# Performance work log

Hardware: AMD Instinct MI355X
Metric: run time of the kernel (lower is better)

Reference implementation:

```python
import jax, jax.numpy as jnp
import numpy as np

B, S, H, E = 64, 1024, 256, 256

def setup_inputs() -> dict:
    key = jax.random.key(0)
    k = jax.random.split(key, 6)
    scale = 1.0 / np.sqrt(H)
    return {
        "data_alpha": jax.random.normal(k[0], (B, S, H), jnp.float32),
        "data_beta": jax.random.normal(k[1], (B, S, H), jnp.float32),
        "data_embed": jax.random.normal(k[2], (B, S, E), jnp.float32),
        "data_mask": jnp.ones((B, S), jnp.float32),
        "Wb": jax.random.normal(k[3], (E, H), jnp.float32) * scale,
        "bb": jnp.zeros((E,), jnp.float32),
        "Wa": jax.random.normal(k[4], (H,), jnp.float32) * scale,
        "ba": jnp.zeros((1,), jnp.float32),
    }

def reference(data_alpha, data_beta, data_embed, data_mask, Wb, bb, Wa, ba):
    # beta gates: tanh(Linear(H->E))  [B,S,E]
    beta_w = jnp.tanh(jnp.einsum('bsh,eh->bse', data_beta, Wb) + bb)
    # alpha logits: Linear(H->1)  [B,S]
    corr = jnp.einsum('bsh,h->bs', data_alpha, Wa) + ba
    attn = jnp.exp(corr)[:, None, :]                       # [B,1,S]
    seq = data_alpha.shape[1]
    flag = jnp.triu(jnp.ones((seq, seq), data_alpha.dtype))[None]  # j >= i
    ef = flag * data_mask[:, None, :]                      # [B,S,S]
    num = attn * ef                                        # [B,S,S]
    acc = jnp.sum(num, axis=-1, keepdims=True) + 1e-10     # [B,S,1]
    alpha = num / acc                                      # [B,S,S]
    ew = beta_w * data_embed                               # [B,S,E]
    return jnp.einsum('bij,bje->bie', alpha, ew)           # [B,S,E]
```

## Files before the change

### kernel.cpp

```cpp
#include <hip/hip_runtime.h>
#include <hip/hip_bf16.h>

#define B_ 64
#define S_ 1024
#define H_ 256
#define E_ 256
#define C_ 16
#define CS_ 64

typedef __attribute__((ext_vector_type(8))) __bf16 bf16x8;
typedef __attribute__((ext_vector_type(4))) __bf16 bf16x4;
typedef __attribute__((ext_vector_type(4))) float f32x4;

__global__ __launch_bounds__(256) void k0_wb_bf16(const float* __restrict__ Wb,
                                                  __bf16* __restrict__ WbBf) {
    int i = blockIdx.x * 256 + threadIdx.x;
    float4 v = ((const float4*)Wb)[i];
    bf16x4 b;
    b[0] = (__bf16)v.x; b[1] = (__bf16)v.y;
    b[2] = (__bf16)v.z; b[3] = (__bf16)v.w;
    ((bf16x4*)WbBf)[i] = b;
}

__global__ __launch_bounds__(256, 4) void k2_fused(
        const float* __restrict__ alpha, const float* __restrict__ beta,
        const float* __restrict__ embed, const float* __restrict__ mask,
        const __bf16* __restrict__ WbBf, const float* __restrict__ bb,
        const float* __restrict__ Wa,    const float* __restrict__ ba,
        float* __restrict__ w, float* __restrict__ chunkTot, float* __restrict__ t) {
    __shared__ float red[4 * E_];
    __shared__ float wsh[CS_];

    const int tid = threadIdx.x;
    const int wv = tid >> 6, lane = tid & 63;
    const int l15 = lane & 15, q = lane >> 4;
    const int m0 = blockIdx.x * CS_;

    {
        const int pr = tid >> 2, pc = tid & 3;
        const int m = m0 + pr;
        const float4* ar = (const float4*)(alpha + (size_t)m * H_ + pc * 64);
        const float4* wr = (const float4*)(Wa + pc * 64);
        float p = 0.f;
        #pragma unroll
        for (int i = 0; i < 16; ++i) {
            float4 a = ar[i], v = wr[i];
            p += a.x * v.x + a.y * v.y + a.z * v.z + a.w * v.w;
        }
        p += __shfl_xor(p, 1, 64);
        p += __shfl_xor(p, 2, 64);
        if (pc == 0) {
            float wm = __expf(p + ba[0]) * mask[m];
            wsh[pr] = wm;
            w[m] = wm;
        }
    }
    __syncthreads();

    const float*  Arow = beta + (size_t)(m0 + wv * 16 + l15) * H_ + q * 8;
    const __bf16* Brow = WbBf + (size_t)l15 * H_ + q * 8;
    f32x4 acc[16];
    #pragma unroll
    for (int i = 0; i < 16; ++i) acc[i] = (f32x4){0.f, 0.f, 0.f, 0.f};

    #pragma unroll 2
    for (int kc = 0; kc < 8; ++kc) {
        float4 a0 = *(const float4*)(Arow + kc * 32);
        float4 a1 = *(const float4*)(Arow + kc * 32 + 4);
        bf16x8 af;
        af[0] = (__bf16)a0.x; af[1] = (__bf16)a0.y;
        af[2] = (__bf16)a0.z; af[3] = (__bf16)a0.w;
        af[4] = (__bf16)a1.x; af[5] = (__bf16)a1.y;
        af[6] = (__bf16)a1.z; af[7] = (__bf16)a1.w;
        #pragma unroll
        for (int et = 0; et < 16; ++et) {
            bf16x8 bf = *(const bf16x8*)(Brow + (size_t)et * 16 * H_ + kc * 32);
            acc[et] = __builtin_amdgcn_mfma_f32_16x16x32_bf16(af, bf, acc[et], 0, 0, 0);
        }
    }

    float wmr[4];
    #pragma unroll
    for (int r = 0; r < 4; ++r) wmr[r] = wsh[wv * 16 + q * 4 + r];

    #pragma unroll
    for (int et = 0; et < 16; ++et) {
        const int e = et * 16 + l15;
        const float bbe = bb[e];
        float tv[4];
        #pragma unroll
        for (int r = 0; r < 4; ++r) {
            const int m = m0 + wv * 16 + q * 4 + r;
            float x = acc[et][r] + bbe;
            x = fminf(fmaxf(x, -15.f), 15.f);
            float ex = __expf(2.f * x);
            float th = (ex - 1.f) / (ex + 1.f);
            tv[r] = wmr[r] * th * embed[(size_t)m * E_ + e];
        }
        float s3 = tv[3];
        float s2 = tv[2] + s3;
        float s1 = tv[1] + s2;
        float s0 = tv[0] + s1;
        float g  = s0;
        float g1 = __shfl_down(g, 16, 64);
        float g2 = __shfl_down(g, 32, 64);
        float g3 = __shfl_down(g, 48, 64);
        float addG = (q < 3 ? g1 : 0.f) + (q < 2 ? g2 : 0.f) + (q < 1 ? g3 : 0.f);
        if (q == 0) red[wv * E_ + e] = g + addG;
        acc[et][0] = s0 + addG;
        acc[et][1] = s1 + addG;
        acc[et][2] = s2 + addG;
        acc[et][3] = s3 + addG;
    }
    __syncthreads();

    #pragma unroll
    for (int et = 0; et < 16; ++et) {
        const int e = et * 16 + l15;
        float wa = 0.f;
        #pragma unroll
        for (int d = 1; d < 4; ++d)
            if (wv + d < 4) wa += red[(wv + d) * E_ + e];
        #pragma unroll
        for (int r = 0; r < 4; ++r) {
            const int m = m0 + wv * 16 + q * 4 + r;
            t[(size_t)m * E_ + e] = acc[et][r] + wa;
        }
    }
    const float ct = red[tid] + red[E_ + tid] + red[2 * E_ + tid] + red[3 * E_ + tid];
    chunkTot[(size_t)blockIdx.x * E_ + tid] = ct;
}

__global__ __launch_bounds__(256) void k3b_scan(
        const float* __restrict__ w, const float* __restrict__ chunkTot,
        float* __restrict__ chunkOff, float* __restrict__ invDen) {
    const int tid = threadIdx.x;
    const int b = blockIdx.x;

    float acc = 0.f;
    #pragma unroll
    for (int c = C_ - 1; c >= 0; --c) {
        chunkOff[((size_t)b * C_ + c) * E_ + tid] = acc;
        acc += chunkTot[((size_t)b * C_ + c) * E_ + tid];
    }

    float4 w4 = *(const float4*)(w + b * S_ + tid * 4);
    float tot = w4.x + w4.y + w4.z + w4.w;
    int lane = tid & 63, wv = tid >> 6;
    float suf = tot;
    #pragma unroll
    for (int off = 1; off < 64; off <<= 1) {
        float o = __shfl_down(suf, off, 64);
        if (lane + off < 64) suf += o;
    }
    __shared__ float wsum[4];
    if (lane == 0) wsum[wv] = suf;
    __syncthreads();
    float waveOff = 0.f;
    for (int j = wv + 1; j < 4; ++j) waveOff += wsum[j];
    float after = (suf - tot) + waveOff;
    float s3 = w4.w + after;
    float s2 = w4.z + s3;
    float s1 = w4.y + s2;
    float s0 = w4.x + s1;
    float4 inv = { 1.f / (s0 + 1e-10f), 1.f / (s1 + 1e-10f),
                   1.f / (s2 + 1e-10f), 1.f / (s3 + 1e-10f) };
    *(float4*)(invDen + b * S_ + tid * 4) = inv;
}

__global__ __launch_bounds__(256) void k3c_finish(
        float* __restrict__ t, const float* __restrict__ chunkOff,
        const float* __restrict__ invDen) {
    const int blk = blockIdx.x;
    const int b = blk >> 4, c = blk & 15;
    const int tid = threadIdx.x;
    float4* tp = (float4*)(t + ((size_t)b * S_ + c * CS_) * E_);
    const float4* co = (const float4*)(chunkOff + (size_t)blk * E_);
    const float* iv = invDen + b * S_ + c * CS_;
    #pragma unroll
    for (int i = 0; i < 16; ++i) {
        const int idx = i * 256 + tid;
        const int row = idx >> 6;
        const int e4 = idx & 63;
        float4 v = tp[idx];
        float4 o = co[e4];
        float s = iv[row];
        v.x = (v.x + o.x) * s;
        v.y = (v.y + o.y) * s;
        v.z = (v.z + o.z) * s;
        v.w = (v.w + o.w) * s;
        tp[idx] = v;
    }
}

extern "C" void kernel_launch(void* const* d_in, const int* in_sizes, int n_in,
                              void* d_out, int out_size, void* d_ws, size_t ws_size,
                              hipStream_t stream) {
    const float* alpha = (const float*)d_in[0];
    const float* beta  = (const float*)d_in[1];
    const float* embed = (const float*)d_in[2];
    const float* mask  = (const float*)d_in[3];
    const float* Wb    = (const float*)d_in[4];
    const float* bb    = (const float*)d_in[5];
    const float* Wa    = (const float*)d_in[6];
    const float* ba    = (const float*)d_in[7];

    float* t = (float*)d_out;

    char* ws = (char*)d_ws;
    float*  w        = (float*)ws;
    float*  chunkTot = (float*)(ws + (256 << 10));
    float*  chunkOff = (float*)(ws + (256 << 10) + (1 << 20));
    float*  invDen   = (float*)(ws + (256 << 10) + (2 << 20));
    __bf16* WbBf     = (__bf16*)(ws + (512 << 10) + (2 << 20));

    k0_wb_bf16<<<E_ * H_ / 1024, 256, 0, stream>>>(Wb, WbBf);
    k2_fused<<<B_ * C_, 256, 0, stream>>>(alpha, beta, embed, mask, WbBf, bb, Wa, ba,
                                          w, chunkTot, t);
    k3b_scan<<<B_, 256, 0, stream>>>(w, chunkTot, chunkOff, invDen);
    k3c_finish<<<B_ * C_, 256, 0, stream>>>(t, chunkOff, invDen);
}
```

Baseline: 303.0 us.

## Fuse scan and finish into cooperative grid-synced kernel, stage Wb in LDS

Makes the main kernel cooperative. After computing per-chunk partial sums it does a grid-wide sync, then computes chunk offsets and denominators locally and writes final outputs directly. This removes the separate scan and finish kernels and the extra read-modify-write of the output. The Wb tiles are also staged through padded LDS per k-chunk instead of being read from global memory by every wave. The cost is a grid barrier, added block syncs in the MFMA loop, and a fallback to the old path if cooperative launch is not supported.

```diff
diff --git a/kernel.cpp b/kernel.cpp
--- a/kernel.cpp
+++ b/kernel.cpp
@@ -1,5 +1,8 @@
 #include <hip/hip_runtime.h>
 #include <hip/hip_bf16.h>
+#include <hip/hip_cooperative_groups.h>
+
+namespace cg = cooperative_groups;
 
 #define B_ 64
 #define S_ 1024
@@ -8,6 +11,8 @@
 #define C_ 16
 #define CS_ 64
 
+#define LDSB_STRIDE 40
+
 typedef __attribute__((ext_vector_type(8))) __bf16 bf16x8;
 typedef __attribute__((ext_vector_type(4))) __bf16 bf16x4;
 typedef __attribute__((ext_vector_type(4))) float f32x4;
@@ -16,25 +21,31 @@
                                                   __bf16* __restrict__ WbBf) {
     int i = blockIdx.x * 256 + threadIdx.x;
     float4 v = ((const float4*)Wb)[i];
-    bf16x4 b;
-    b[0] = (__bf16)v.x; b[1] = (__bf16)v.y;
-    b[2] = (__bf16)v.z; b[3] = (__bf16)v.w;
-    ((bf16x4*)WbBf)[i] = b;
-}
-
-__global__ __launch_bounds__(256, 4) void k2_fused(
+    bf16x4 bv;
+    bv[0] = (__bf16)v.x; bv[1] = (__bf16)v.y;
+    bv[2] = (__bf16)v.z; bv[3] = (__bf16)v.w;
+    ((bf16x4*)WbBf)[i] = bv;
+}
+
+template <bool COOP>
+__global__ __launch_bounds__(256, 4) void k2_main(
         const float* __restrict__ alpha, const float* __restrict__ beta,
         const float* __restrict__ embed, const float* __restrict__ mask,
         const __bf16* __restrict__ WbBf, const float* __restrict__ bb,
         const float* __restrict__ Wa,    const float* __restrict__ ba,
-        float* __restrict__ w, float* __restrict__ chunkTot, float* __restrict__ t) {
+        float* __restrict__ chunkTot, float* __restrict__ wChunkSum,
+        float* __restrict__ w, float* __restrict__ t) {
+    __shared__ __bf16 ldsB[E_ * LDSB_STRIDE];
     __shared__ float red[4 * E_];
     __shared__ float wsh[CS_];
+    __shared__ float wsuf[CS_];
 
     const int tid = threadIdx.x;
     const int wv = tid >> 6, lane = tid & 63;
     const int l15 = lane & 15, q = lane >> 4;
-    const int m0 = blockIdx.x * CS_;
+    const int blk = blockIdx.x;
+    const int bat = blk >> 4, c = blk & 15;
+    const int m0 = blk * CS_;
 
     {
         const int pr = tid >> 2, pc = tid & 3;
@@ -52,21 +63,39 @@
         if (pc == 0) {
             float wm = __expf(p + ba[0]) * mask[m];
             wsh[pr] = wm;
-            w[m] = wm;
+            if constexpr (!COOP) w[m] = wm;
         }
     }
     __syncthreads();
-
-    const float*  Arow = beta + (size_t)(m0 + wv * 16 + l15) * H_ + q * 8;
-    const __bf16* Brow = WbBf + (size_t)l15 * H_ + q * 8;
+    if constexpr (COOP) {
+        if (tid < 64) {
+            float v = wsh[tid];
+            #pragma unroll
+            for (int off = 32; off; off >>= 1) v += __shfl_xor(v, off, 64);
+            if (tid == 0) wChunkSum[blk] = v;
+        }
+    }
+
+    const float* Arow = beta + (size_t)(m0 + wv * 16 + l15) * H_ + q * 8;
     f32x4 acc[16];
     #pragma unroll
     for (int i = 0; i < 16; ++i) acc[i] = (f32x4){0.f, 0.f, 0.f, 0.f};
 
-    #pragma unroll 2
+    const int se = tid >> 2;
+    const int sk = (tid & 3) * 8;
+
     for (int kc = 0; kc < 8; ++kc) {
         float4 a0 = *(const float4*)(Arow + kc * 32);
         float4 a1 = *(const float4*)(Arow + kc * 32 + 4);
+
+        #pragma unroll
+        for (int pass = 0; pass < 4; ++pass) {
+            int e = pass * 64 + se;
+            bf16x8 bv = *(const bf16x8*)(WbBf + (size_t)e * H_ + kc * 32 + sk);
+            *(bf16x8*)(ldsB + e * LDSB_STRIDE + sk) = bv;
+        }
+        __syncthreads();
+
         bf16x8 af;
         af[0] = (__bf16)a0.x; af[1] = (__bf16)a0.y;
         af[2] = (__bf16)a0.z; af[3] = (__bf16)a0.w;
@@ -74,9 +103,10 @@
         af[6] = (__bf16)a1.z; af[7] = (__bf16)a1.w;
         #pragma unroll
         for (int et = 0; et < 16; ++et) {
-            bf16x8 bf = *(const bf16x8*)(Brow + (size_t)et * 16 * H_ + kc * 32);
+            bf16x8 bf = *(const bf16x8*)(ldsB + (et * 16 + l15) * LDSB_STRIDE + q * 8);
             acc[et] = __builtin_amdgcn_mfma_f32_16x16x32_bf16(af, bf, acc[et], 0, 0, 0);
         }
+        __syncthreads();
     }
 
     float wmr[4];
@@ -114,21 +144,70 @@
     }
     __syncthreads();
 
+    const float ct = red[tid] + red[E_ + tid] + red[2 * E_ + tid] + red[3 * E_ + tid];
+    chunkTot[(size_t)blk * E_ + tid] = ct;
     #pragma unroll
     for (int et = 0; et < 16; ++et) {
         const int e = et * 16 + l15;
         float wa = 0.f;
-        #pragma unroll
-        for (int d = 1; d < 4; ++d)
-            if (wv + d < 4) wa += red[(wv + d) * E_ + e];
-        #pragma unroll
-        for (int r = 0; r < 4; ++r) {
-            const int m = m0 + wv * 16 + q * 4 + r;
-            t[(size_t)m * E_ + e] = acc[et][r] + wa;
-        }
-    }
-    const float ct = red[tid] + red[E_ + tid] + red[2 * E_ + tid] + red[3 * E_ + tid];
-    chunkTot[(size_t)blockIdx.x * E_ + tid] = ct;
+        if (wv < 3) wa += red[(wv + 1) * E_ + e];
+        if (wv < 2) wa += red[(wv + 2) * E_ + e];
+        if (wv < 1) wa += red[(wv + 3) * E_ + e];
+        acc[et][0] += wa; acc[et][1] += wa;
+        acc[et][2] += wa; acc[et][3] += wa;
+    }
+
+    if constexpr (!COOP) {
+        #pragma unroll
+        for (int et = 0; et < 16; ++et) {
+            const int e = et * 16 + l15;
+            #pragma unroll
+            for (int r = 0; r < 4; ++r) {
+                const int m = m0 + wv * 16 + q * 4 + r;
+                t[(size_t)m * E_ + e] = acc[et][r];
+            }
+        }
+        return;
+    } else {
+        __threadfence();
+        cg::this_grid().sync();
+        __threadfence();
+
+        float off = 0.f;
+        for (int cc = c + 1; cc < C_; ++cc)
+            off += chunkTot[((size_t)(bat * C_ + cc)) * E_ + tid];
+        red[tid] = off;
+
+        float wtail = 0.f;
+        for (int cc = c + 1; cc < C_; ++cc)
+            wtail += wChunkSum[bat * C_ + cc];
+
+        if (tid < 64) wsuf[tid] = wsh[tid];
+        __syncthreads();
+        for (int d = 1; d < 64; d <<= 1) {
+            float v = 0.f;
+            if (tid < 64 && tid + d < 64) v = wsuf[tid + d];
+            __syncthreads();
+            if (tid < 64) wsuf[tid] += v;
+            __syncthreads();
+        }
+
+        float inv[4];
+        #pragma unroll
+        for (int r = 0; r < 4; ++r)
+            inv[r] = 1.f / (wsuf[wv * 16 + q * 4 + r] + wtail + 1e-10f);
+
+        #pragma unroll
+        for (int et = 0; et < 16; ++et) {
+            const int e = et * 16 + l15;
+            const float oe = red[e];
+            #pragma unroll
+            for (int r = 0; r < 4; ++r) {
+                const int m = m0 + wv * 16 + q * 4 + r;
+                t[(size_t)m * E_ + e] = (acc[et][r] + oe) * inv[r];
+            }
+        }
+    }
 }
 
 __global__ __launch_bounds__(256) void k3b_scan(
@@ -193,6 +272,8 @@
     }
 }
 
+static int g_coop = -1;
+
 extern "C" void kernel_launch(void* const* d_in, const int* in_sizes, int n_in,
                               void* d_out, int out_size, void* d_ws, size_t ws_size,
                               hipStream_t stream) {
@@ -201,22 +282,44 @@
     const float* embed = (const float*)d_in[2];
     const float* mask  = (const float*)d_in[3];
     const float* Wb    = (const float*)d_in[4];
-    const float* bb    = (const float*)d_in[5];
+    const float* bbp   = (const float*)d_in[5];
     const float* Wa    = (const float*)d_in[6];
-    const float* ba    = (const float*)d_in[7];
+    const float* bap   = (const float*)d_in[7];
 
     float* t = (float*)d_out;
 
     char* ws = (char*)d_ws;
-    float*  w        = (float*)ws;
-    float*  chunkTot = (float*)(ws + (256 << 10));
-    float*  chunkOff = (float*)(ws + (256 << 10) + (1 << 20));
-    float*  invDen   = (float*)(ws + (256 << 10) + (2 << 20));
-    __bf16* WbBf     = (__bf16*)(ws + (512 << 10) + (2 << 20));
+    float*  chunkTot  = (float*)ws;
+    float*  wChunkSum = (float*)(ws + (1 << 20));
+    float*  w         = (float*)(ws + (1 << 20) + (16 << 10));
+    float*  chunkOff  = (float*)(ws + (1 << 20) + (16 << 10) + (256 << 10));
+    float*  invDen    = (float*)(ws + (2 << 20) + (16 << 10) + (256 << 10));
+    __bf16* WbBf      = (__bf16*)(ws + (2 << 20) + (16 << 10) + (512 << 10));
+
+    if (g_coop < 0) {
+        int dev = 0;
+        hipGetDevice(&dev);
+        int attr = 0;
+        hipDeviceGetAttribute(&attr, hipDeviceAttributeCooperativeLaunch, dev);
+        int nb = 0;
+        hipOccupancyMaxActiveBlocksPerMultiprocessor(&nb, k2_main<true>, 256, 0);
+        g_coop = (attr != 0 && nb >= 4) ? 1 : 0;
+    }
 
     k0_wb_bf16<<<E_ * H_ / 1024, 256, 0, stream>>>(Wb, WbBf);
-    k2_fused<<<B_ * C_, 256, 0, stream>>>(alpha, beta, embed, mask, WbBf, bb, Wa, ba,
-                                          w, chunkTot, t);
+
+    if (g_coop == 1) {
+        void* args[] = { (void*)&alpha, (void*)&beta, (void*)&embed, (void*)&mask,
+                         (void*)&WbBf, (void*)&bbp, (void*)&Wa, (void*)&bap,
+                         (void*)&chunkTot, (void*)&wChunkSum, (void*)&w, (void*)&t };
+        hipError_t e = hipLaunchCooperativeKernel(k2_main<true>, dim3(B_ * C_),
+                                                  dim3(256), args, 0u, stream);
+        if (e == hipSuccess) return;
+        g_coop = 0;
+    }
+
+    k2_main<false><<<B_ * C_, 256, 0, stream>>>(alpha, beta, embed, mask, WbBf, bbp,
+                                                Wa, bap, chunkTot, wChunkSum, w, t);
     k3b_scan<<<B_, 256, 0, stream>>>(w, chunkTot, chunkOff, invDen);
     k3c_finish<<<B_ * C_, 256, 0, stream>>>(t, chunkOff, invDen);
 }
```

Measured after the change: 262.6 us. 13.3% less time.

## Fuse chunk scan and normalization into main kernel with per-E-group sequential sweep

Applied to the files above, without the earlier changes.

Restructures the pipeline into two kernels. A prep kernel now computes the exp-logit weights alongside the Wb bf16 conversion. The main kernel assigns each block one batch and a 32-wide E slice and walks the sequence chunks from end to start, carrying the running suffix sum in LDS. It computes the denominator scan in-block and writes the final normalized output directly. This removes the chunk totals/offsets buffers, the separate scan kernel, and the extra read-modify-write pass over the output. In exchange, beta is re-read once per E group, relying on cache to absorb it. Each block also processes its chunks serially with barriers, which reduces the parallelism available inside a block.

```diff
diff --git a/kernel.cpp b/kernel.cpp
--- a/kernel.cpp
+++ b/kernel.cpp
@@ -5,191 +5,213 @@
 #define S_ 1024
 #define H_ 256
 #define E_ 256
-#define C_ 16
-#define CS_ 64
+
+#define EG_ 32
+#define LDSB_ST 264
+#define CH_ 128
+#define NCH_ 8
 
 typedef __attribute__((ext_vector_type(8))) __bf16 bf16x8;
 typedef __attribute__((ext_vector_type(4))) __bf16 bf16x4;
 typedef __attribute__((ext_vector_type(4))) float f32x4;
 
-__global__ __launch_bounds__(256) void k0_wb_bf16(const float* __restrict__ Wb,
-                                                  __bf16* __restrict__ WbBf) {
-    int i = blockIdx.x * 256 + threadIdx.x;
-    float4 v = ((const float4*)Wb)[i];
-    bf16x4 b;
-    b[0] = (__bf16)v.x; b[1] = (__bf16)v.y;
-    b[2] = (__bf16)v.z; b[3] = (__bf16)v.w;
-    ((bf16x4*)WbBf)[i] = b;
+__global__ __launch_bounds__(256) void k0_prep(
+        const float* __restrict__ alpha, const float* __restrict__ mask,
+        const float* __restrict__ Wa,    const float* __restrict__ ba,
+        const float* __restrict__ Wb,    __bf16* __restrict__ WbBf,
+        float* __restrict__ w) {
+    const int tid = threadIdx.x, blk = blockIdx.x;
+    if (blk < 64) {
+        int i = blk * 256 + tid;
+        float4 v = ((const float4*)Wb)[i];
+        bf16x4 bv;
+        bv[0] = (__bf16)v.x; bv[1] = (__bf16)v.y;
+        bv[2] = (__bf16)v.z; bv[3] = (__bf16)v.w;
+        ((bf16x4*)WbBf)[i] = bv;
+    }
+    const int pr = tid >> 2, pc = tid & 3;
+    const int m = blk * 64 + pr;
+    const float4* ar = (const float4*)(alpha + (size_t)m * H_ + pc * 64);
+    const float4* wr = (const float4*)(Wa + pc * 64);
+    float p = 0.f;
+    #pragma unroll
+    for (int i = 0; i < 16; ++i) {
+        float4 a = ar[i], v = wr[i];
+        p += a.x * v.x + a.y * v.y + a.z * v.z + a.w * v.w;
+    }
+    p += __shfl_xor(p, 1, 64);
+    p += __shfl_xor(p, 2, 64);
+    if (pc == 0) w[m] = __expf(p + ba[0]) * mask[m];
 }
 
-__global__ __launch_bounds__(256, 4) void k2_fused(
-        const float* __restrict__ alpha, const float* __restrict__ beta,
-        const float* __restrict__ embed, const float* __restrict__ mask,
+__global__ __launch_bounds__(512, 4) void k2_main(
+        const float* __restrict__ beta, const float* __restrict__ embed,
         const __bf16* __restrict__ WbBf, const float* __restrict__ bb,
-        const float* __restrict__ Wa,    const float* __restrict__ ba,
-        float* __restrict__ w, float* __restrict__ chunkTot, float* __restrict__ t) {
-    __shared__ float red[4 * E_];
-    __shared__ float wsh[CS_];
+        const float* __restrict__ w, float* __restrict__ t) {
+    __shared__ __bf16 ldsB[EG_ * LDSB_ST];
+    __shared__ float wsLds[S_];
+    __shared__ float ivLds[S_];
+    __shared__ float red[8 * EG_];
+    __shared__ float run[EG_];
+    __shared__ float wsum[4];
 
     const int tid = threadIdx.x;
     const int wv = tid >> 6, lane = tid & 63;
     const int l15 = lane & 15, q = lane >> 4;
-    const int m0 = blockIdx.x * CS_;
-
+    const int blk = blockIdx.x;
+    const int b  = (blk & 7) * 8 + (blk >> 6);
+    const int eg = (blk >> 3) & 7;
+
+    if (tid < 256)
+        *(float4*)(wsLds + tid * 4) = *(const float4*)(w + b * S_ + tid * 4);
     {
-        const int pr = tid >> 2, pc = tid & 3;
-        const int m = m0 + pr;
-        const float4* ar = (const float4*)(alpha + (size_t)m * H_ + pc * 64);
-        const float4* wr = (const float4*)(Wa + pc * 64);
-        float p = 0.f;
+        const int e = tid >> 4, ks = (tid & 15) * 16;
+        const __bf16* src = WbBf + (size_t)(eg * EG_ + e) * H_ + ks;
+        *(bf16x8*)(ldsB + e * LDSB_ST + ks)     = *(const bf16x8*)(src);
+        *(bf16x8*)(ldsB + e * LDSB_ST + ks + 8) = *(const bf16x8*)(src + 8);
+    }
+    if (tid < EG_) run[tid] = 0.f;
+    __syncthreads();
+
+    {
+        float w0 = 0, w1 = 0, w2 = 0, w3 = 0, tot = 0, suf = 0;
+        const int sl = tid & 63, sw = tid >> 6;
+        if (tid < 256) {
+            w0 = wsLds[tid * 4];     w1 = wsLds[tid * 4 + 1];
+            w2 = wsLds[tid * 4 + 2]; w3 = wsLds[tid * 4 + 3];
+            tot = w0 + w1 + w2 + w3;
+            suf = tot;
+            #pragma unroll
+            for (int off = 1; off < 64; off <<= 1) {
+                float o = __shfl_down(suf, off, 64);
+                if (sl + off < 64) suf += o;
+            }
+            if (sl == 0) wsum[sw] = suf;
+        }
+        __syncthreads();
+        if (tid < 256) {
+            float waveOff = 0.f;
+            for (int j = sw + 1; j < 4; ++j) waveOff += wsum[j];
+            float after = (suf - tot) + waveOff;
+            float s3 = w3 + after, s2 = w2 + s3, s1 = w1 + s2, s0 = w0 + s1;
+            ivLds[tid * 4]     = 1.f / (s0 + 1e-10f);
+            ivLds[tid * 4 + 1] = 1.f / (s1 + 1e-10f);
+            ivLds[tid * 4 + 2] = 1.f / (s2 + 1e-10f);
+            ivLds[tid * 4 + 3] = 1.f / (s3 + 1e-10f);
+        }
+        __syncthreads();
+    }
+
+    const float bb0 = bb[eg * EG_ + l15];
+    const float bb1 = bb[eg * EG_ + 16 + l15];
+
+    for (int c = NCH_ - 1; c >= 0; --c) {
+        const int rbase = c * CH_ + wv * 16;
+        const float* Ar = beta + (size_t)(b * S_ + rbase + l15) * H_ + q * 8;
+
+        f32x4 acc0 = {0.f, 0.f, 0.f, 0.f}, acc1 = {0.f, 0.f, 0.f, 0.f};
         #pragma unroll
-        for (int i = 0; i < 16; ++i) {
-            float4 a = ar[i], v = wr[i];
-            p += a.x * v.x + a.y * v.y + a.z * v.z + a.w * v.w;
-        }
-        p += __shfl_xor(p, 1, 64);
-        p += __shfl_xor(p, 2, 64);
-        if (pc == 0) {
-            float wm = __expf(p + ba[0]) * mask[m];
-            wsh[pr] = wm;
-            w[m] = wm;
-        }
-    }
-    __syncthreads();
-
-    const float*  Arow = beta + (size_t)(m0 + wv * 16 + l15) * H_ + q * 8;
-    const __bf16* Brow = WbBf + (size_t)l15 * H_ + q * 8;
-    f32x4 acc[16];
-    #pragma unroll
-    for (int i = 0; i < 16; ++i) acc[i] = (f32x4){0.f, 0.f, 0.f, 0.f};
-
-    #pragma unroll 2
-    for (int kc = 0; kc < 8; ++kc) {
-        float4 a0 = *(const float4*)(Arow + kc * 32);
-        float4 a1 = *(const float4*)(Arow + kc * 32 + 4);
-        bf16x8 af;
-        af[0] = (__bf16)a0.x; af[1] = (__bf16)a0.y;
-        af[2] = (__bf16)a0.z; af[3] = (__bf16)a0.w;
-        af[4] = (__bf16)a1.x; af[5] = (__bf16)a1.y;
-        af[6] = (__bf16)a1.z; af[7] = (__bf16)a1.w;
-        #pragma unroll
-        for (int et = 0; et < 16; ++et) {
-            bf16x8 bf = *(const bf16x8*)(Brow + (size_t)et * 16 * H_ + kc * 32);
-            acc[et] = __builtin_amdgcn_mfma_f32_16x16x32_bf16(af, bf, acc[et], 0, 0, 0);
-        }
-    }
-
-    float wmr[4];
-    #pragma unroll
-    for (int r = 0; r < 4; ++r) wmr[r] = wsh[wv * 16 + q * 4 + r];
-
-    #pragma unroll
-    for (int et = 0; et < 16; ++et) {
-        const int e = et * 16 + l15;
-        const float bbe = bb[e];
-        float tv[4];
-        #pragma unroll
-        for (int r = 0; r < 4; ++r) {
-            const int m = m0 + wv * 16 + q * 4 + r;
-            float x = acc[et][r] + bbe;
-            x = fminf(fmaxf(x, -15.f), 15.f);
-            float ex = __expf(2.f * x);
-            float th = (ex - 1.f) / (ex + 1.f);
-            tv[r] = wmr[r] * th * embed[(size_t)m * E_ + e];
-        }
-        float s3 = tv[3];
-        float s2 = tv[2] + s3;
-        float s1 = tv[1] + s2;
-        float s0 = tv[0] + s1;
-        float g  = s0;
-        float g1 = __shfl_down(g, 16, 64);
-        float g2 = __shfl_down(g, 32, 64);
-        float g3 = __shfl_down(g, 48, 64);
-        float addG = (q < 3 ? g1 : 0.f) + (q < 2 ? g2 : 0.f) + (q < 1 ? g3 : 0.f);
-        if (q == 0) red[wv * E_ + e] = g + addG;
-        acc[et][0] = s0 + addG;
-        acc[et][1] = s1 + addG;
-        acc[et][2] = s2 + addG;
-        acc[et][3] = s3 + addG;
-    }
-    __syncthreads();
-
-    #pragma unroll
-    for (int et = 0; et < 16; ++et) {
-        const int e = et * 16 + l15;
-        float wa = 0.f;
-        #pragma unroll
-        for (int d = 1; d < 4; ++d)
-            if (wv + d < 4) wa += red[(wv + d) * E_ + e];
-        #pragma unroll
-        for (int r = 0; r < 4; ++r) {
-            const int m = m0 + wv * 16 + q * 4 + r;
-            t[(size_t)m * E_ + e] = acc[et][r] + wa;
-        }
-    }
-    const float ct = red[tid] + red[E_ + tid] + red[2 * E_ + tid] + red[3 * E_ + tid];
-    chunkTot[(size_t)blockIdx.x * E_ + tid] = ct;
-}
-
-__global__ __launch_bounds__(256) void k3b_scan(
-        const float* __restrict__ w, const float* __restrict__ chunkTot,
-        float* __restrict__ chunkOff, float* __restrict__ invDen) {
-    const int tid = threadIdx.x;
-    const int b = blockIdx.x;
-
-    float acc = 0.f;
-    #pragma unroll
-    for (int c = C_ - 1; c >= 0; --c) {
-        chunkOff[((size_t)b * C_ + c) * E_ + tid] = acc;
-        acc += chunkTot[((size_t)b * C_ + c) * E_ + tid];
-    }
-
-    float4 w4 = *(const float4*)(w + b * S_ + tid * 4);
-    float tot = w4.x + w4.y + w4.z + w4.w;
-    int lane = tid & 63, wv = tid >> 6;
-    float suf = tot;
-    #pragma unroll
-    for (int off = 1; off < 64; off <<= 1) {
-        float o = __shfl_down(suf, off, 64);
-        if (lane + off < 64) suf += o;
-    }
-    __shared__ float wsum[4];
-    if (lane == 0) wsum[wv] = suf;
-    __syncthreads();
-    float waveOff = 0.f;
-    for (int j = wv + 1; j < 4; ++j) waveOff += wsum[j];
-    float after = (suf - tot) + waveOff;
-    float s3 = w4.w + after;
-    float s2 = w4.z + s3;
-    float s1 = w4.y + s2;
-    float s0 = w4.x + s1;
-    float4 inv = { 1.f / (s0 + 1e-10f), 1.f / (s1 + 1e-10f),
-                   1.f / (s2 + 1e-10f), 1.f / (s3 + 1e-10f) };
-    *(float4*)(invDen + b * S_ + tid * 4) = inv;
-}
-
-__global__ __launch_bounds__(256) void k3c_finish(
-        float* __restrict__ t, const float* __restrict__ chunkOff,
-        const float* __restrict__ invDen) {
-    const int blk = blockIdx.x;
-    const int b = blk >> 4, c = blk & 15;
-    const int tid = threadIdx.x;
-    float4* tp = (float4*)(t + ((size_t)b * S_ + c * CS_) * E_);
-    const float4* co = (const float4*)(chunkOff + (size_t)blk * E_);
-    const float* iv = invDen + b * S_ + c * CS_;
-    #pragma unroll
-    for (int i = 0; i < 16; ++i) {
-        const int idx = i * 256 + tid;
-        const int row = idx >> 6;
-        const int e4 = idx & 63;
-        float4 v = tp[idx];
-        float4 o = co[e4];
-        float s = iv[row];
-        v.x = (v.x + o.x) * s;
-        v.y = (v.y + o.y) * s;
-        v.z = (v.z + o.z) * s;
-        v.w = (v.w + o.w) * s;
-        tp[idx] = v;
+        for (int kc = 0; kc < 8; ++kc) {
+            float4 a0 = *(const float4*)(Ar + kc * 32);
+            float4 a1 = *(const float4*)(Ar + kc * 32 + 4);
+            bf16x8 af;
+            af[0] = (__bf16)a0.x; af[1] = (__bf16)a0.y;
+            af[2] = (__bf16)a0.z; af[3] = (__bf16)a0.w;
+            af[4] = (__bf16)a1.x; af[5] = (__bf16)a1.y;
+            af[6] = (__bf16)a1.z; af[7] = (__bf16)a1.w;
+            bf16x8 bf0 = *(const bf16x8*)(ldsB + l15 * LDSB_ST + kc * 32 + q * 8);
+            bf16x8 bf1 = *(const bf16x8*)(ldsB + (16 + l15) * LDSB_ST + kc * 32 + q * 8);
+            acc0 = __builtin_amdgcn_mfma_f32_16x16x32_bf16(af, bf0, acc0, 0, 0, 0);
+            acc1 = __builtin_amdgcn_mfma_f32_16x16x32_bf16(af, bf1, acc1, 0, 0, 0);
+        }
+
+        float sv0[4], sv1[4];
+        {
+            const int eG = eg * EG_ + l15;
+            float tv[4];
+            #pragma unroll
+            for (int r = 0; r < 4; ++r) {
+                const int m = c * CH_ + wv * 16 + q * 4 + r;
+                float x = acc0[r] + bb0;
+                x = fminf(fmaxf(x, -15.f), 15.f);
+                float ex = __expf(2.f * x);
+                float th = (ex - 1.f) / (ex + 1.f);
+                tv[r] = wsLds[m] * th * embed[(size_t)(b * S_ + m) * E_ + eG];
+            }
+            float s3 = tv[3], s2 = tv[2] + s3, s1 = tv[1] + s2, s0 = tv[0] + s1;
+            float g = s0;
+            float g1 = __shfl_down(g, 16, 64);
+            float g2 = __shfl_down(g, 32, 64);
+            float g3 = __shfl_down(g, 48, 64);
+            float addG = (q < 3 ? g1 : 0.f) + (q < 2 ? g2 : 0.f) + (q < 1 ? g3 : 0.f);
+            if (q == 0) red[wv * EG_ + l15] = g + addG;
+            sv0[0] = s0 + addG; sv0[1] = s1 + addG;
+            sv0[2] = s2 + addG; sv0[3] = s3 + addG;
+        }
+        {
+            const int eG = eg * EG_ + 16 + l15;
+            float tv[4];
+            #pragma unroll
+            for (int r = 0; r < 4; ++r) {
+                const int m = c * CH_ + wv * 16 + q * 4 + r;
+                float x = acc1[r] + bb1;
+                x = fminf(fmaxf(x, -15.f), 15.f);
+                float ex = __expf(2.f * x);
+                float th = (ex - 1.f) / (ex + 1.f);
+                tv[r] = wsLds[m] * th * embed[(size_t)(b * S_ + m) * E_ + eG];
+            }
+            float s3 = tv[3], s2 = tv[2] + s3, s1 = tv[1] + s2, s0 = tv[0] + s1;
+            float g = s0;
+            float g1 = __shfl_down(g, 16, 64);
+            float g2 = __shfl_down(g, 32, 64);
+            float g3 = __shfl_down(g, 48, 64);
+            float addG = (q < 3 ? g1 : 0.f) + (q < 2 ? g2 : 0.f) + (q < 1 ? g3 : 0.f);
+            if (q == 0) red[wv * EG_ + 16 + l15] = g + addG;
+            sv1[0] = s0 + addG; sv1[1] = s1 + addG;
+            sv1[2] = s2 + addG; sv1[3] = s3 + addG;
+        }
+        __syncthreads();
+
+        float nr0 = 0.f, nr1 = 0.f;
+        {
+            const int eG = eg * EG_ + l15;
+            const float rn = run[l15];
+            float later = rn, tot = 0.f;
+            #pragma unroll
+            for (int w2 = 0; w2 < 8; ++w2) {
+                float v = red[w2 * EG_ + l15];
+                tot += v;
+                if (w2 > wv) later += v;
+            }
+            nr0 = rn + tot;
+            #pragma unroll
+            for (int r = 0; r < 4; ++r) {
+                const int m = c * CH_ + wv * 16 + q * 4 + r;
+                t[(size_t)(b * S_ + m) * E_ + eG] = (sv0[r] + later) * ivLds[m];
+            }
+        }
+        {
+            const int eG = eg * EG_ + 16 + l15;
+            const float rn = run[16 + l15];
+            float later = rn, tot = 0.f;
+            #pragma unroll
+            for (int w2 = 0; w2 < 8; ++w2) {
+                float v = red[w2 * EG_ + 16 + l15];
+                tot += v;
+                if (w2 > wv) later += v;
+            }
+            nr1 = rn + tot;
+            #pragma unroll
+            for (int r = 0; r < 4; ++r) {
+                const int m = c * CH_ + wv * 16 + q * 4 + r;
+                t[(size_t)(b * S_ + m) * E_ + eG] = (sv1[r] + later) * ivLds[m];
+            }
+        }
+        __syncthreads();
+        if (wv == 0 && q == 0) {
+            run[l15] = nr0;
+            run[16 + l15] = nr1;
+        }
     }
 }
 
@@ -201,22 +223,16 @@
     const float* embed = (const float*)d_in[2];
     const float* mask  = (const float*)d_in[3];
     const float* Wb    = (const float*)d_in[4];
-    const float* bb    = (const float*)d_in[5];
+    const float* bbp   = (const float*)d_in[5];
     const float* Wa    = (const float*)d_in[6];
-    const float* ba    = (const float*)d_in[7];
+    const float* bap   = (const float*)d_in[7];
 
     float* t = (float*)d_out;
 
     char* ws = (char*)d_ws;
-    float*  w        = (float*)ws;
-    float*  chunkTot = (float*)(ws + (256 << 10));
-    float*  chunkOff = (float*)(ws + (256 << 10) + (1 << 20));
-    float*  invDen   = (float*)(ws + (256 << 10) + (2 << 20));
-    __bf16* WbBf     = (__bf16*)(ws + (512 << 10) + (2 << 20));
-
-    k0_wb_bf16<<<E_ * H_ / 1024, 256, 0, stream>>>(Wb, WbBf);
-    k2_fused<<<B_ * C_, 256, 0, stream>>>(alpha, beta, embed, mask, WbBf, bb, Wa, ba,
-                                          w, chunkTot, t);
-    k3b_scan<<<B_, 256, 0, stream>>>(w, chunkTot, chunkOff, invDen);
-    k3c_finish<<<B_ * C_, 256, 0, stream>>>(t, chunkOff, invDen);
+    float*  w    = (float*)ws;
+    __bf16* WbBf = (__bf16*)(ws + (256 << 10));
+
+    k0_prep<<<B_ * S_ / 64, 256, 0, stream>>>(alpha, mask, Wa, bap, Wb, WbBf, w);
+    k2_main<<<B_ * (E_ / EG_), 512, 0, stream>>>(beta, embed, WbBf, bbp, w, t);
 }
```

After: 279.0 us. 7.9% less time.
